# Kernel tuning notes

Hardware: AMD Instinct MI355X
Metric: run time of the kernel (lower is better)

Reference implementation:

```python
import jax, jax.numpy as jnp
import numpy as np

N_NODES = 100000
N_EDGES = 1600000
IN_DIM, HID_DIM, OUT_DIM = 128, 128, 64
BN_EPS = 1e-5


def _norm_edges(edge_index, n):
    # PyG GCNConv: add self-loops, symmetric normalization deg^-1/2
    loop = jnp.arange(n, dtype=edge_index.dtype)
    src = jnp.concatenate([edge_index[0], loop])
    dst = jnp.concatenate([edge_index[1], loop])
    deg = jax.ops.segment_sum(jnp.ones_like(dst, dtype=jnp.float32), dst, num_segments=n)
    dinv = jnp.where(deg > 0, jax.lax.rsqrt(deg), 0.0)
    norm = dinv[src] * dinv[dst]  # [E+N]
    return src, dst, norm


def _gcn_conv(x, src, dst, norm, W, b):
    h = x @ W                      # [N, d_out]
    msg = h[src] * norm[:, None]   # [E+N, d_out] gather + scale
    out = jax.ops.segment_sum(msg, dst, num_segments=x.shape[0])  # scatter-add
    return out + b


def _bn(x, g, be):
    mu = x.mean(axis=0)
    var = x.var(axis=0)
    return (x - mu) * jax.lax.rsqrt(var + BN_EPS) * g + be


def setup_inputs() -> dict:
    key = jax.random.key(0)
    ks = jax.random.split(key, 6)
    s1 = (1.0 / np.sqrt(IN_DIM)).astype(np.float32)
    s2 = (1.0 / np.sqrt(HID_DIM)).astype(np.float32)
    return {
        "x": jax.random.normal(ks[0], (N_NODES, IN_DIM), dtype=jnp.float32),
        "edge_index": jax.random.randint(ks[1], (2, N_EDGES), 0, N_NODES, dtype=jnp.int32),
        "W1": jax.random.normal(ks[2], (IN_DIM, HID_DIM), dtype=jnp.float32) * s1,
        "b1": jnp.zeros((HID_DIM,), jnp.float32),
        "g1": jnp.ones((HID_DIM,), jnp.float32),
        "be1": jnp.zeros((HID_DIM,), jnp.float32),
        "W2": jax.random.normal(ks[3], (HID_DIM, HID_DIM), dtype=jnp.float32) * s2,
        "b2": jnp.zeros((HID_DIM,), jnp.float32),
        "g2": jnp.ones((HID_DIM,), jnp.float32),
        "be2": jnp.zeros((HID_DIM,), jnp.float32),
        "W3": jax.random.normal(ks[4], (HID_DIM, OUT_DIM), dtype=jnp.float32) * s2,
        "b3": jnp.zeros((OUT_DIM,), jnp.float32),
    }


def reference(x, edge_index, W1, b1, g1, be1, W2, b2, g2, be2, W3, b3):
    src, dst, norm = _norm_edges(edge_index, x.shape[0])
    h = jax.nn.relu(_bn(_gcn_conv(x, src, dst, norm, W1, b1), g1, be1))
    h = jax.nn.relu(_bn(_gcn_conv(h, src, dst, norm, W2, b2), g2, be2))
    return _gcn_conv(h, src, dst, norm, W3, b3)
```

## Files before the change

### kernel.cpp

```cpp
#include <hip/hip_runtime.h>

#define N_NODES 100000
#define N_EDGES 1600000
#define PAD 48
#define NB 391
#define NBLK 256
#define EPB (N_EDGES / NBLK)
#define SCAN_N (NB * NBLK)

using bf16x8 = __attribute__((ext_vector_type(8))) short;
using f32x4  = __attribute__((ext_vector_type(4))) float;


__device__ __forceinline__ float bflo(unsigned u) { return __uint_as_float(u << 16); }
__device__ __forceinline__ float bfhi(unsigned u) { return __uint_as_float(u & 0xffff0000u); }
__device__ __forceinline__ unsigned packbf(float a, float b) {
    unsigned ua = __float_as_uint(a), ub = __float_as_uint(b);
    ua = ua + 0x7fffu + ((ua >> 16) & 1u);
    ub = ub + 0x7fffu + ((ub >> 16) & 1u);
    return (ua >> 16) | (ub & 0xffff0000u);
}


__global__ void statsinit_kernel(float* __restrict__ s1, float* __restrict__ s2) {
    int i = threadIdx.x;
    s1[i] = 0.f;
    s2[i] = 0.f;
}

__global__ __launch_bounds__(256) void hist_kernel(const int* __restrict__ dst,
                                                   int* __restrict__ counts) {
    __shared__ int hist[NB];
    int tid = threadIdx.x, blk = blockIdx.x;
    for (int i = tid; i < NB; i += 256) hist[i] = 0;
    __syncthreads();
    int s0 = blk * EPB;
    for (int k = tid; k < EPB; k += 256)
        atomicAdd(&hist[dst[s0 + k] >> 8], 1);
    __syncthreads();
    for (int b = tid; b < NB; b += 256) counts[b * NBLK + blk] = hist[b];
}

__global__ __launch_bounds__(1024) void scan1_kernel(const int* __restrict__ cnt,
                                                     int* __restrict__ off,
                                                     int* __restrict__ bsum, int n) {
    __shared__ int wsum[17];
    int tid = threadIdx.x, lane = tid & 63, w = tid >> 6;
    int i = blockIdx.x * 1024 + tid;
    int v = (i < n) ? cnt[i] : 0;
    int x = v;
    #pragma unroll
    for (int d = 1; d < 64; d <<= 1) {
        int y = __shfl_up(x, d, 64);
        if (lane >= d) x += y;
    }
    if (lane == 63) wsum[w] = x;
    __syncthreads();
    if (tid == 0) {
        int s = 0;
        #pragma unroll
        for (int j = 0; j < 16; j++) { int t = wsum[j]; wsum[j] = s; s += t; }
        wsum[16] = s;
    }
    __syncthreads();
    if (i < n) off[i + 1] = x + wsum[w];
    if (tid == 0) bsum[blockIdx.x] = wsum[16];
}

__global__ void scan2_kernel(int* __restrict__ bsum, int nb) {
    if (threadIdx.x == 0) {
        int s = 0;
        for (int j = 0; j < nb; j++) { int t = bsum[j]; bsum[j] = s; s += t; }
    }
}

__global__ __launch_bounds__(1024) void scan3_kernel(int* __restrict__ off,
                                                     const int* __restrict__ bsum, int n) {
    int i = blockIdx.x * 1024 + threadIdx.x;
    if (i < n) off[i + 1] += bsum[blockIdx.x];
    if (i == 0) off[0] = 0;
}

__global__ __launch_bounds__(256) void part_kernel(const int* __restrict__ src,
                                                   const int* __restrict__ dst,
                                                   const int* __restrict__ off,
                                                   int2* __restrict__ ebuf) {
    __shared__ int cur[NB];
    int tid = threadIdx.x, blk = blockIdx.x;
    for (int b = tid; b < NB; b += 256) cur[b] = off[b * NBLK + blk];
    __syncthreads();
    int s0 = blk * EPB;
    for (int k = tid; k < EPB; k += 256) {
        int s = src[s0 + k], d = dst[s0 + k];
        int pos = atomicAdd(&cur[d >> 8], 1);
        ebuf[pos] = make_int2(s, d);
    }
}

__global__ __launch_bounds__(256) void bucket_kernel(const int2* __restrict__ ebuf,
                                                     const int* __restrict__ off,
                                                     int* __restrict__ esrc_pad,
                                                     int* __restrict__ cnt,
                                                     float* __restrict__ dinv, int n) {
    __shared__ int epad[256 * PAD];
    __shared__ int cur[256];
    int tid = threadIdx.x, b = blockIdx.x;
    int start = off[b * NBLK], end = off[(b + 1) * NBLK];
    cur[tid] = 0;
    __syncthreads();
    for (int e = start + tid; e < end; e += 256) {
        int2 sd = ebuf[e];
        int ld = sd.y & 255;
        int pos = atomicAdd(&cur[ld], 1);
        if (pos < PAD) epad[ld * PAD + pos] = sd.x;
    }
    __syncthreads();
    int nd0 = b << 8;
    int nn = min(256, n - nd0);
    if (tid < nn) {
        cnt[nd0 + tid] = cur[tid];
        dinv[nd0 + tid] = rsqrtf((float)(cur[tid] + 1));
    }
    int tot = nn * PAD;
    for (int i = tid; i < tot; i += 256) esrc_pad[(size_t)nd0 * PAD + i] = epad[i];
}


__global__ void wconv3_kernel(const float* __restrict__ W1, const float* __restrict__ W2,
                              const float* __restrict__ W3, unsigned* __restrict__ Wt1,
                              unsigned* __restrict__ Wt2, unsigned* __restrict__ Wt3) {
    int b = blockIdx.x;
    const float* W;
    unsigned* Wt;
    int M, i;
    if (b < 32)      { W = W1; Wt = Wt1; M = 128; i = b * 256 + threadIdx.x; }
    else if (b < 64) { W = W2; Wt = Wt2; M = 128; i = (b - 32) * 256 + threadIdx.x; }
    else             { W = W3; Wt = Wt3; M = 64;  i = (b - 64) * 256 + threadIdx.x; }
    if (i >= M * 64) return;
    int m = i >> 6, ku = i & 63;
    Wt[(size_t)m * 64 + ku] = packbf(W[(size_t)(2 * ku) * M + m], W[(size_t)(2 * ku + 1) * M + m]);
}


template <int M, int MODE>
__global__ __launch_bounds__(256) void gemm_mfma_kernel(const void* __restrict__ Xv,
                                                        const unsigned* __restrict__ Wt,
                                                        const float* __restrict__ ss,
                                                        unsigned* __restrict__ H, int n) {
    int wid = threadIdx.x >> 6, lane = threadIdx.x & 63;
    int r0 = (blockIdx.x * 4 + wid) * 16;
    if (r0 >= n) return;
    int rl = lane & 15, kg = lane >> 4;
    int row = r0 + rl;

    bf16x8 xf[4];
    if constexpr (MODE == 0) {
        const float* X = (const float*)Xv;
        #pragma unroll
        for (int ks = 0; ks < 4; ks++) {
            const float* p = &X[(size_t)row * 128 + ks * 32 + kg * 8];
            float4 f0 = *(const float4*)p;
            float4 f1 = *(const float4*)(p + 4);
            unsigned o[4] = { packbf(f0.x, f0.y), packbf(f0.z, f0.w),
                              packbf(f1.x, f1.y), packbf(f1.z, f1.w) };
            xf[ks] = *(bf16x8*)o;
        }
    } else {
        const unsigned* X = (const unsigned*)Xv;
        #pragma unroll
        for (int ks = 0; ks < 4; ks++) {
            int c = ks * 32 + kg * 8;
            uint4 u = *(const uint4*)&X[(size_t)row * 64 + (c >> 1)];
            float4 sc0 = *(const float4*)&ss[c];
            float4 sc1 = *(const float4*)&ss[c + 4];
            float4 sh0 = *(const float4*)&ss[128 + c];
            float4 sh1 = *(const float4*)&ss[128 + c + 4];
            float v0 = fmaxf(bflo(u.x) * sc0.x + sh0.x, 0.f);
            float v1 = fmaxf(bfhi(u.x) * sc0.y + sh0.y, 0.f);
            float v2 = fmaxf(bflo(u.y) * sc0.z + sh0.z, 0.f);
            float v3 = fmaxf(bfhi(u.y) * sc0.w + sh0.w, 0.f);
            float v4 = fmaxf(bflo(u.z) * sc1.x + sh1.x, 0.f);
            float v5 = fmaxf(bfhi(u.z) * sc1.y + sh1.y, 0.f);
            float v6 = fmaxf(bflo(u.w) * sc1.z + sh1.z, 0.f);
            float v7 = fmaxf(bfhi(u.w) * sc1.w + sh1.w, 0.f);
            unsigned o[4] = { packbf(v0, v1), packbf(v2, v3), packbf(v4, v5), packbf(v6, v7) };
            xf[ks] = *(bf16x8*)o;
        }
    }

    constexpr int NCB = M / 16;
    f32x4 acc[NCB];
    #pragma unroll
    for (int cb = 0; cb < NCB; cb++) acc[cb] = (f32x4){0.f, 0.f, 0.f, 0.f};

    #pragma unroll
    for (int cb = 0; cb < NCB; cb++) {
        #pragma unroll
        for (int ks = 0; ks < 4; ks++) {
            bf16x8 wf = *(const bf16x8*)&Wt[(size_t)(cb * 16 + rl) * 64 + ks * 16 + kg * 4];
            acc[cb] = __builtin_amdgcn_mfma_f32_16x16x32_bf16(wf, xf[ks], acc[cb], 0, 0, 0);
        }
    }

    unsigned* Hrow = &H[(size_t)row * (M / 2)];
    #pragma unroll
    for (int cb = 0; cb < NCB; cb++) {
        uint2 o;
        o.x = packbf(acc[cb][0], acc[cb][1]);
        o.y = packbf(acc[cb][2], acc[cb][3]);
        *(uint2*)&Hrow[cb * 8 + kg * 2] = o;
    }
}


__global__ __launch_bounds__(256) void agg128_kernel(const unsigned* __restrict__ H,
                                                     const int* __restrict__ cnt,
                                                     const int* __restrict__ esrc_pad,
                                                     const float* __restrict__ dinv,
                                                     const float* __restrict__ bias,
                                                     unsigned* __restrict__ out, int n) {
    int node = (blockIdx.x * blockDim.x + threadIdx.x) >> 6;
    int lane = threadIdx.x & 63;
    if (node >= n) return;
    float dn = dinv[node];
    float2 b = *(const float2*)&bias[lane * 2];
    int c = min(cnt[node], PAD);
    int s_l = (lane < c) ? esrc_pad[(size_t)node * PAD + lane] : node;
    float w_l = (lane < c) ? dinv[s_l] * dn : 0.f;
    unsigned u0 = H[(size_t)node * 64 + lane];
    float acc0 = dn * dn * bflo(u0), acc1 = dn * dn * bfhi(u0);
    for (int j = 0; j < c; j += 16) {
        unsigned u[16];
        int sr[16];
        float wr[16];
        #pragma unroll
        for (int t = 0; t < 16; t++) {
            sr[t] = __builtin_amdgcn_readlane(s_l, j + t);
            wr[t] = __uint_as_float(__builtin_amdgcn_readlane(__float_as_uint(w_l), j + t));
            u[t] = H[(size_t)sr[t] * 64 + lane];
        }
        #pragma unroll
        for (int t = 0; t < 16; t++) {
            acc0 += wr[t] * bflo(u[t]);
            acc1 += wr[t] * bfhi(u[t]);
        }
    }
    out[(size_t)node * 64 + lane] = packbf(acc0 + b.x, acc1 + b.y);
}

__global__ __launch_bounds__(256) void agg64_kernel(const unsigned short* __restrict__ H,
                                                    const int* __restrict__ cnt,
                                                    const int* __restrict__ esrc_pad,
                                                    const float* __restrict__ dinv,
                                                    const float* __restrict__ bias,
                                                    float* __restrict__ out, int n) {
    int node = (blockIdx.x * blockDim.x + threadIdx.x) >> 6;
    int lane = threadIdx.x & 63;
    if (node >= n) return;
    float dn = dinv[node];
    float bb = bias[lane];
    int c = min(cnt[node], PAD);
    int s_l = (lane < c) ? esrc_pad[(size_t)node * PAD + lane] : node;
    float w_l = (lane < c) ? dinv[s_l] * dn : 0.f;
    float acc = dn * dn * __uint_as_float(((unsigned)H[(size_t)node * 64 + lane]) << 16);
    for (int j = 0; j < c; j += 16) {
        unsigned short u[16];
        int sr[16];
        float wr[16];
        #pragma unroll
        for (int t = 0; t < 16; t++) {
            sr[t] = __builtin_amdgcn_readlane(s_l, j + t);
            wr[t] = __uint_as_float(__builtin_amdgcn_readlane(__float_as_uint(w_l), j + t));
            u[t] = H[(size_t)sr[t] * 64 + lane];
        }
        #pragma unroll
        for (int t = 0; t < 16; t++) {
            acc += wr[t] * __uint_as_float(((unsigned)u[t]) << 16);
        }
    }
    out[(size_t)node * 64 + lane] = acc + bb;
}


__global__ __launch_bounds__(256) void bnstats_kernel(const unsigned* __restrict__ X,
                                                      float* __restrict__ stats, int n) {
    int tid = threadIdx.x;
    int cpair = (tid & 31) * 2;
    int c0 = cpair * 2;
    int rg = tid >> 5;
    float s0 = 0, s1 = 0, s2 = 0, s3 = 0, q0 = 0, q1 = 0, q2 = 0, q3 = 0;
    int r0 = blockIdx.x * 512;
    int rend = min(r0 + 512, n);
    for (int r = r0 + rg; r < rend; r += 8) {
        uint2 u = *(const uint2*)&X[(size_t)r * 64 + cpair];
        float f0 = bflo(u.x), f1 = bfhi(u.x), f2 = bflo(u.y), f3 = bfhi(u.y);
        s0 += f0; q0 += f0 * f0;
        s1 += f1; q1 += f1 * f1;
        s2 += f2; q2 += f2 * f2;
        s3 += f3; q3 += f3 * f3;
    }
    __shared__ float ls[8][128], lq[8][128];
    ls[rg][c0] = s0; ls[rg][c0 + 1] = s1; ls[rg][c0 + 2] = s2; ls[rg][c0 + 3] = s3;
    lq[rg][c0] = q0; lq[rg][c0 + 1] = q1; lq[rg][c0 + 2] = q2; lq[rg][c0 + 3] = q3;
    __syncthreads();
    if (tid < 128) {
        float s = 0, q = 0;
        #pragma unroll
        for (int j = 0; j < 8; j++) { s += ls[j][tid]; q += lq[j][tid]; }
        atomicAdd(&stats[tid], s);
        atomicAdd(&stats[128 + tid], q);
    }
}

__global__ void bnscale_kernel(const float* __restrict__ stats, const float* __restrict__ g,
                               const float* __restrict__ be, float* __restrict__ ss, int n) {
    int c = threadIdx.x;
    float inv_n = 1.f / (float)n;
    float mu = stats[c] * inv_n;
    float var = stats[128 + c] * inv_n - mu * mu;
    float sc = g[c] * rsqrtf(var + 1e-5f);
    ss[c] = sc;
    ss[128 + c] = be[c] - mu * sc;
}


extern "C" void kernel_launch(void* const* d_in, const int* in_sizes, int n_in,
                              void* d_out, int out_size, void* d_ws, size_t ws_size,
                              hipStream_t stream) {
    const float* x  = (const float*)d_in[0];
    const int*   ei = (const int*)d_in[1];
    const float* W1 = (const float*)d_in[2];
    const float* b1 = (const float*)d_in[3];
    const float* g1 = (const float*)d_in[4];
    const float* be1 = (const float*)d_in[5];
    const float* W2 = (const float*)d_in[6];
    const float* b2 = (const float*)d_in[7];
    const float* g2 = (const float*)d_in[8];
    const float* be2 = (const float*)d_in[9];
    const float* W3 = (const float*)d_in[10];
    const float* b3 = (const float*)d_in[11];
    float* out = (float*)d_out;

    const int n = N_NODES, E = N_EDGES;
    const int* src = ei;
    const int* dst = ei + E;
    const int gemmGrid = (n + 63) / 64;
    const int nbScan = (SCAN_N + 1023) / 1024;

    char* p = (char*)d_ws;
    auto alloc = [&](size_t bytes) {
        void* r = (void*)p;
        p += (bytes + 255) & ~(size_t)255;
        return r;
    };
    int*      counts   = (int*)alloc((size_t)SCAN_N * 4);
    int*      off      = (int*)alloc((size_t)(SCAN_N + 1) * 4);
    int*      bsum     = (int*)alloc((size_t)nbScan * 4);
    int2*     ebuf     = (int2*)alloc((size_t)E * 8);
    int*      cnt      = (int*)alloc((size_t)n * 4);
    float*    dinv     = (float*)alloc((size_t)n * 4);
    int*      esrc_pad = (int*)alloc((size_t)n * PAD * 4);
    unsigned* Hb       = (unsigned*)alloc((size_t)n * 64 * 4);
    unsigned* Ab       = (unsigned*)alloc((size_t)n * 64 * 4);
    unsigned* Wt1      = (unsigned*)alloc(128 * 64 * 4);
    unsigned* Wt2      = (unsigned*)alloc(128 * 64 * 4);
    unsigned* Wt3      = (unsigned*)alloc(64 * 64 * 4);
    float*    stats1   = (float*)alloc(256 * 4);
    float*    stats2   = (float*)alloc(256 * 4);
    float*    ss1      = (float*)alloc(256 * 4);
    float*    ss2      = (float*)alloc(256 * 4);

    statsinit_kernel<<<1, 256, 0, stream>>>(stats1, stats2);
    hist_kernel<<<NBLK, 256, 0, stream>>>(dst, counts);
    scan1_kernel<<<nbScan, 1024, 0, stream>>>(counts, off, bsum, SCAN_N);
    scan2_kernel<<<1, 64, 0, stream>>>(bsum, nbScan);
    scan3_kernel<<<nbScan, 1024, 0, stream>>>(off, bsum, SCAN_N);
    part_kernel<<<NBLK, 256, 0, stream>>>(src, dst, off, ebuf);
    bucket_kernel<<<NB, 256, 0, stream>>>(ebuf, off, esrc_pad, cnt, dinv, n);

    wconv3_kernel<<<80, 256, 0, stream>>>(W1, W2, W3, Wt1, Wt2, Wt3);

    gemm_mfma_kernel<128, 0><<<gemmGrid, 256, 0, stream>>>(x, Wt1, nullptr, Hb, n);
    agg128_kernel<<<n / 4, 256, 0, stream>>>(Hb, cnt, esrc_pad, dinv, b1, Ab, n);
    bnstats_kernel<<<(n + 511) / 512, 256, 0, stream>>>(Ab, stats1, n);
    bnscale_kernel<<<1, 128, 0, stream>>>(stats1, g1, be1, ss1, n);

    gemm_mfma_kernel<128, 1><<<gemmGrid, 256, 0, stream>>>(Ab, Wt2, ss1, Hb, n);
    agg128_kernel<<<n / 4, 256, 0, stream>>>(Hb, cnt, esrc_pad, dinv, b2, Ab, n);
    bnstats_kernel<<<(n + 511) / 512, 256, 0, stream>>>(Ab, stats2, n);
    bnscale_kernel<<<1, 128, 0, stream>>>(stats2, g2, be2, ss2, n);

    gemm_mfma_kernel<64, 1><<<gemmGrid, 256, 0, stream>>>(Ab, Wt3, ss2, Hb, n);
    agg64_kernel<<<n / 4, 256, 0, stream>>>((const unsigned short*)Hb, cnt, esrc_pad, dinv, b3, out, n);
}
```

Baseline: 378.2 us.

## Fuse batch-norm statistics and scale computation into the aggregation kernel

The 128-wide aggregation kernel now accumulates per-channel sum and sum-of-squares from its fp32 outputs, then atomically adds them to global stats. A last-block counter computes the BN scale/shift, which removes the separate bnstats and bnscale launches and a re-read of the aggregated activations. The kernel becomes grid-stride with a fixed 2048-block grid, and stats zeroing moves into scan2. Statistics now come from the unrounded fp32 values rather than the bf16-rounded ones, and the last-block pattern relies on fences and atomics for ordering.

```diff
diff --git a/kernel.cpp b/kernel.cpp
--- a/kernel.cpp
+++ b/kernel.cpp
@@ -7,6 +7,7 @@
 #define NBLK 256
 #define EPB (N_EDGES / NBLK)
 #define SCAN_N (NB * NBLK)
+#define AGG_GRID 2048
 
 using bf16x8 = __attribute__((ext_vector_type(8))) short;
 using f32x4  = __attribute__((ext_vector_type(4))) float;
@@ -21,12 +22,6 @@
     return (ua >> 16) | (ub & 0xffff0000u);
 }
 
-
-__global__ void statsinit_kernel(float* __restrict__ s1, float* __restrict__ s2) {
-    int i = threadIdx.x;
-    s1[i] = 0.f;
-    s2[i] = 0.f;
-}
 
 __global__ __launch_bounds__(256) void hist_kernel(const int* __restrict__ dst,
                                                    int* __restrict__ counts) {
@@ -67,10 +62,15 @@
     if (tid == 0) bsum[blockIdx.x] = wsum[16];
 }
 
-__global__ void scan2_kernel(int* __restrict__ bsum, int nb) {
-    if (threadIdx.x == 0) {
+__global__ void scan2_kernel(int* __restrict__ bsum, int nb, float* __restrict__ stats1,
+                             float* __restrict__ stats2, int* __restrict__ ctr) {
+    int t = threadIdx.x;
+    stats1[t] = 0.f;
+    stats2[t] = 0.f;
+    if (t < 2) ctr[t] = 0;
+    if (t == 0) {
         int s = 0;
-        for (int j = 0; j < nb; j++) { int t = bsum[j]; bsum[j] = s; s += t; }
+        for (int j = 0; j < nb; j++) { int v = bsum[j]; bsum[j] = s; s += v; }
     }
 }
 
@@ -213,39 +213,76 @@
 }
 
 
-__global__ __launch_bounds__(256) void agg128_kernel(const unsigned* __restrict__ H,
-                                                     const int* __restrict__ cnt,
-                                                     const int* __restrict__ esrc_pad,
-                                                     const float* __restrict__ dinv,
-                                                     const float* __restrict__ bias,
-                                                     unsigned* __restrict__ out, int n) {
-    int node = (blockIdx.x * blockDim.x + threadIdx.x) >> 6;
+__global__ __launch_bounds__(256) void agg128bn_kernel(const unsigned* __restrict__ H,
+                                                       const int* __restrict__ cnt,
+                                                       const int* __restrict__ esrc_pad,
+                                                       const float* __restrict__ dinv,
+                                                       const float* __restrict__ bias,
+                                                       unsigned* __restrict__ out,
+                                                       float* __restrict__ stats,
+                                                       float* __restrict__ ss,
+                                                       const float* __restrict__ g,
+                                                       const float* __restrict__ be,
+                                                       int* __restrict__ counter, int n) {
     int lane = threadIdx.x & 63;
-    if (node >= n) return;
-    float dn = dinv[node];
+    int wv = threadIdx.x >> 6;
+    int gw = blockIdx.x * 4 + wv;
     float2 b = *(const float2*)&bias[lane * 2];
-    int c = min(cnt[node], PAD);
-    int s_l = (lane < c) ? esrc_pad[(size_t)node * PAD + lane] : node;
-    float w_l = (lane < c) ? dinv[s_l] * dn : 0.f;
-    unsigned u0 = H[(size_t)node * 64 + lane];
-    float acc0 = dn * dn * bflo(u0), acc1 = dn * dn * bfhi(u0);
-    for (int j = 0; j < c; j += 16) {
-        unsigned u[16];
-        int sr[16];
-        float wr[16];
-        #pragma unroll
-        for (int t = 0; t < 16; t++) {
-            sr[t] = __builtin_amdgcn_readlane(s_l, j + t);
-            wr[t] = __uint_as_float(__builtin_amdgcn_readlane(__float_as_uint(w_l), j + t));
-            u[t] = H[(size_t)sr[t] * 64 + lane];
-        }
-        #pragma unroll
-        for (int t = 0; t < 16; t++) {
-            acc0 += wr[t] * bflo(u[t]);
-            acc1 += wr[t] * bfhi(u[t]);
-        }
-    }
-    out[(size_t)node * 64 + lane] = packbf(acc0 + b.x, acc1 + b.y);
+    float s0 = 0.f, s1 = 0.f, q0 = 0.f, q1 = 0.f;
+    for (int node = gw; node < n; node += AGG_GRID * 4) {
+        float dn = dinv[node];
+        int c = min(cnt[node], PAD);
+        int s_l = (lane < c) ? esrc_pad[(size_t)node * PAD + lane] : node;
+        float w_l = (lane < c) ? dinv[s_l] * dn : 0.f;
+        unsigned u0 = H[(size_t)node * 64 + lane];
+        float acc0 = dn * dn * bflo(u0), acc1 = dn * dn * bfhi(u0);
+        for (int j = 0; j < c; j += 16) {
+            unsigned u[16];
+            int sr[16];
+            float wr[16];
+            #pragma unroll
+            for (int t = 0; t < 16; t++) {
+                sr[t] = __builtin_amdgcn_readlane(s_l, j + t);
+                wr[t] = __uint_as_float(__builtin_amdgcn_readlane(__float_as_uint(w_l), j + t));
+                u[t] = H[(size_t)sr[t] * 64 + lane];
+            }
+            #pragma unroll
+            for (int t = 0; t < 16; t++) {
+                acc0 += wr[t] * bflo(u[t]);
+                acc1 += wr[t] * bfhi(u[t]);
+            }
+        }
+        float o0 = acc0 + b.x, o1 = acc1 + b.y;
+        out[(size_t)node * 64 + lane] = packbf(o0, o1);
+        s0 += o0; q0 += o0 * o0;
+        s1 += o1; q1 += o1 * o1;
+    }
+    __shared__ float ls[4][128], lq[4][128];
+    ls[wv][lane * 2] = s0; ls[wv][lane * 2 + 1] = s1;
+    lq[wv][lane * 2] = q0; lq[wv][lane * 2 + 1] = q1;
+    __syncthreads();
+    int tid = threadIdx.x;
+    if (tid < 128) {
+        float s = ls[0][tid] + ls[1][tid] + ls[2][tid] + ls[3][tid];
+        float q = lq[0][tid] + lq[1][tid] + lq[2][tid] + lq[3][tid];
+        atomicAdd(&stats[tid], s);
+        atomicAdd(&stats[128 + tid], q);
+    }
+    __syncthreads();
+    __threadfence();
+    __shared__ int isLast;
+    if (tid == 0) isLast = (atomicAdd(counter, 1) == (int)gridDim.x - 1);
+    __syncthreads();
+    if (isLast && tid < 128) {
+        float s = atomicAdd(&stats[tid], 0.f);
+        float q = atomicAdd(&stats[128 + tid], 0.f);
+        float inv_n = 1.f / (float)n;
+        float mu = s * inv_n;
+        float var = q * inv_n - mu * mu;
+        float sc = g[tid] * rsqrtf(var + 1e-5f);
+        ss[tid] = sc;
+        ss[128 + tid] = be[tid] - mu * sc;
+    }
 }
 
 __global__ __launch_bounds__(256) void agg64_kernel(const unsigned short* __restrict__ H,
@@ -279,48 +316,6 @@
         }
     }
     out[(size_t)node * 64 + lane] = acc + bb;
-}
-
-
-__global__ __launch_bounds__(256) void bnstats_kernel(const unsigned* __restrict__ X,
-                                                      float* __restrict__ stats, int n) {
-    int tid = threadIdx.x;
-    int cpair = (tid & 31) * 2;
-    int c0 = cpair * 2;
-    int rg = tid >> 5;
-    float s0 = 0, s1 = 0, s2 = 0, s3 = 0, q0 = 0, q1 = 0, q2 = 0, q3 = 0;
-    int r0 = blockIdx.x * 512;
-    int rend = min(r0 + 512, n);
-    for (int r = r0 + rg; r < rend; r += 8) {
-        uint2 u = *(const uint2*)&X[(size_t)r * 64 + cpair];
-        float f0 = bflo(u.x), f1 = bfhi(u.x), f2 = bflo(u.y), f3 = bfhi(u.y);
-        s0 += f0; q0 += f0 * f0;
-        s1 += f1; q1 += f1 * f1;
-        s2 += f2; q2 += f2 * f2;
-        s3 += f3; q3 += f3 * f3;
-    }
-    __shared__ float ls[8][128], lq[8][128];
-    ls[rg][c0] = s0; ls[rg][c0 + 1] = s1; ls[rg][c0 + 2] = s2; ls[rg][c0 + 3] = s3;
-    lq[rg][c0] = q0; lq[rg][c0 + 1] = q1; lq[rg][c0 + 2] = q2; lq[rg][c0 + 3] = q3;
-    __syncthreads();
-    if (tid < 128) {
-        float s = 0, q = 0;
-        #pragma unroll
-        for (int j = 0; j < 8; j++) { s += ls[j][tid]; q += lq[j][tid]; }
-        atomicAdd(&stats[tid], s);
-        atomicAdd(&stats[128 + tid], q);
-    }
-}
-
-__global__ void bnscale_kernel(const float* __restrict__ stats, const float* __restrict__ g,
-                               const float* __restrict__ be, float* __restrict__ ss, int n) {
-    int c = threadIdx.x;
-    float inv_n = 1.f / (float)n;
-    float mu = stats[c] * inv_n;
-    float var = stats[128 + c] * inv_n - mu * mu;
-    float sc = g[c] * rsqrtf(var + 1e-5f);
-    ss[c] = sc;
-    ss[128 + c] = be[c] - mu * sc;
 }
 
 
@@ -369,11 +364,11 @@
     float*    stats2   = (float*)alloc(256 * 4);
     float*    ss1      = (float*)alloc(256 * 4);
     float*    ss2      = (float*)alloc(256 * 4);
-
-    statsinit_kernel<<<1, 256, 0, stream>>>(stats1, stats2);
+    int*      ctr      = (int*)alloc(2 * 4);
+
     hist_kernel<<<NBLK, 256, 0, stream>>>(dst, counts);
     scan1_kernel<<<nbScan, 1024, 0, stream>>>(counts, off, bsum, SCAN_N);
-    scan2_kernel<<<1, 64, 0, stream>>>(bsum, nbScan);
+    scan2_kernel<<<1, 256, 0, stream>>>(bsum, nbScan, stats1, stats2, ctr);
     scan3_kernel<<<nbScan, 1024, 0, stream>>>(off, bsum, SCAN_N);
     part_kernel<<<NBLK, 256, 0, stream>>>(src, dst, off, ebuf);
     bucket_kernel<<<NB, 256, 0, stream>>>(ebuf, off, esrc_pad, cnt, dinv, n);
@@ -381,14 +376,12 @@
     wconv3_kernel<<<80, 256, 0, stream>>>(W1, W2, W3, Wt1, Wt2, Wt3);
 
     gemm_mfma_kernel<128, 0><<<gemmGrid, 256, 0, stream>>>(x, Wt1, nullptr, Hb, n);
-    agg128_kernel<<<n / 4, 256, 0, stream>>>(Hb, cnt, esrc_pad, dinv, b1, Ab, n);
-    bnstats_kernel<<<(n + 511) / 512, 256, 0, stream>>>(Ab, stats1, n);
-    bnscale_kernel<<<1, 128, 0, stream>>>(stats1, g1, be1, ss1, n);
+    agg128bn_kernel<<<AGG_GRID, 256, 0, stream>>>(Hb, cnt, esrc_pad, dinv, b1, Ab,
+                                                  stats1, ss1, g1, be1, &ctr[0], n);
 
     gemm_mfma_kernel<128, 1><<<gemmGrid, 256, 0, stream>>>(Ab, Wt2, ss1, Hb, n);
-    agg128_kernel<<<n / 4, 256, 0, stream>>>(Hb, cnt, esrc_pad, dinv, b2, Ab, n);
-    bnstats_kernel<<<(n + 511) / 512, 256, 0, stream>>>(Ab, stats2, n);
-    bnscale_kernel<<<1, 128, 0, stream>>>(stats2, g2, be2, ss2, n);
+    agg128bn_kernel<<<AGG_GRID, 256, 0, stream>>>(Hb, cnt, esrc_pad, dinv, b2, Ab,
+                                                  stats2, ss2, g2, be2, &ctr[1], n);
 
     gemm_mfma_kernel<64, 1><<<gemmGrid, 256, 0, stream>>>(Ab, Wt3, ss2, Hb, n);
     agg64_kernel<<<n / 4, 256, 0, stream>>>((const unsigned short*)Hb, cnt, esrc_pad, dinv, b3, out, n);
```

Result: slower. 760.7 us (+101.1%).
